# Kernel optimization log

Measured on AMD Instinct MI355X. Metric: run time of the kernel, lower is better.

The kernel has to match this reference:

```python
import jax, jax.numpy as jnp
import numpy as np

B, T, H, K = 128, 32, 256, 32


def setup_inputs() -> dict:
    key = jax.random.key(0)
    ks = jax.random.split(key, 24)
    s = 0.02  # small weight scale keeps exp(pdf) stable

    def n(k, shape, scale=s):
        return jax.random.normal(k, shape, dtype=jnp.float32) * scale

    inp = {
        "input_encoded": jax.random.normal(ks[0], (B, T, H), dtype=jnp.float32),
        "y_prev": jax.random.normal(ks[1], (B, T), dtype=jnp.float32),
        "attn_W1": n(ks[2], (H, 3 * H)),
        "attn_b1": n(ks[3], (H,)),
        "attn_W2": n(ks[4], (1, H)),
        "attn_b2": n(ks[5], (1,)),
        "fc_W": n(ks[6], (1, H + 1)),
        "fc_b": n(ks[7], (1,)),
        "var_W": n(ks[8], (H, H + 1)),
        "var_b": n(ks[9], (H,)),
        "W_ih": n(ks[10], (4 * H, 1)),
        "W_hh": n(ks[11], (4 * H, H)),
        "b_ih": n(ks[12], (4 * H,)),
        "b_hh": n(ks[13], (4 * H,)),
        "fc_dec_W": n(ks[14], (1, H)),
        "fc_dec_b": n(ks[15], (1,)),
        "pdf_W": n(ks[16], (1, H + 1)),
        "pdf_b": n(ks[17], (1,)),
        "fc_enc_W": n(ks[18], (1, H)),
        "fc_enc_b": n(ks[19], (1,)),
        "num_particles": K,
    }
    return inp


def reference(input_encoded, y_prev, attn_W1, attn_b1, attn_W2, attn_b2,
              fc_W, fc_b, var_W, var_b, W_ih, W_hh, b_ih, b_hh,
              fc_dec_W, fc_dec_b, pdf_W, pdf_b, fc_enc_W, fc_enc_b,
              num_particles):
    Bn, Tn, Hn = input_encoded.shape
    Kn = num_particles
    base = jax.random.key(42)
    arB = jnp.arange(Bn)

    def step(carry, xs):
        hiddens, cells = carry  # each (K*B, H), flat index = k*B + b
        t, y_t = xs  # y_t: (B,)
        k1, k2 = jax.random.split(jax.random.fold_in(base, t))
        # particle means (torch: mean over dim 0 of (K, B, H) view)
        hm = hiddens.reshape(Kn, Bn, Hn).mean(axis=0)  # (B, H)
        cm = cells.reshape(Kn, Bn, Hn).mean(axis=0)
        # attention over encoder timesteps
        x = jnp.concatenate([
            jnp.broadcast_to(hm[:, None, :], (Bn, Tn, Hn)),
            jnp.broadcast_to(cm[:, None, :], (Bn, Tn, Hn)),
            input_encoded], axis=2)  # (B, T, 3H)
        a = jnp.tanh(x @ attn_W1.T + attn_b1) @ attn_W2.T + attn_b2  # (B, T, 1)
        beta = jax.nn.softmax(a[..., 0], axis=1)  # (B, T)
        context = jnp.einsum('bt,bth->bh', beta, input_encoded)  # (B, H)
        y_tilde = jnp.concatenate([context, y_t[:, None]], axis=1) @ fc_W.T + fc_b  # (B, 1)
        var = jnp.concatenate([y_tilde, hm], axis=1) @ var_W.T + var_b  # (B, H)
        # single-step LSTM cell over all particles (torch gate order i,f,g,o)
        x_in = jnp.tile(y_tilde, (Kn, 1))  # (K*B, 1)
        gates = x_in @ W_ih.T + b_ih + hiddens @ W_hh.T + b_hh  # (K*B, 4H)
        i, f, g, o = jnp.split(gates, 4, axis=1)
        c_new = jax.nn.sigmoid(f) * cells + jax.nn.sigmoid(i) * jnp.tanh(g)
        h_new = jax.nn.sigmoid(o) * jnp.tanh(c_new)
        # reparameterization: h = mu + eps * softplus(var)
        std = jnp.tile(jax.nn.softplus(var), (Kn, 1))  # (K*B, H)
        eps = jax.random.normal(k1, (Kn * Bn, Hn), dtype=h_new.dtype)
        h_new = h_new + eps * std
        # sort_hidden: per-batch argsort of 1-d projection, gather hiddens only
        proj = h_new @ fc_dec_W.T + fc_dec_b  # (K*B, 1)
        idx = jnp.argsort(proj.reshape(Kn, Bn).T, axis=1)  # (B, K)
        flat = (arB[:, None] + idx * Bn).T.reshape(-1)  # (K*B,)
        h_sorted = h_new[flat]
        # particle weights (replicates torch's view(-1, K, 1) reshape exactly)
        y = jnp.concatenate([h_sorted, jnp.tile(y_tilde, (Kn, 1))], axis=1)
        prob = jnp.exp(y @ pdf_W.T + pdf_b).reshape(Bn, Kn, 1)
        prob = prob / prob.sum(axis=1, keepdims=True)
        # soft-resampling: multinomial over (B, K) rows (torch: prob.view(K,-1).T)
        logits = jnp.log(prob.reshape(Kn, Bn).T)  # (B, K)
        samp = jax.random.categorical(k2, logits, shape=(Kn, Bn))  # (K, B)
        flat2 = (samp * Bn + arB[None, :]).reshape(-1)
        return (h_sorted[flat2], c_new[flat2]), context

    h0 = jnp.zeros((Kn * Bn, Hn), dtype=input_encoded.dtype)
    (hiddens, _), contexts = jax.lax.scan(step, (h0, h0), (jnp.arange(Tn), y_prev.T))
    context = contexts[-1]
    hm = hiddens.reshape(Kn, Bn, Hn).mean(axis=0)  # (B, H)
    y_pred = hm @ fc_dec_W.T + fc_dec_b + context @ fc_enc_W.T + fc_enc_b  # (B, 1)
    return y_pred
```

## Files before the change

kernel.cpp:

```cpp
#include <hip/hip_runtime.h>
#include <cstdint>


#define Bn 128
#define Tn 32
#define Hn 256
#define Kn 32

__host__ __device__ inline void tf2x32(uint32_t k0, uint32_t k1, uint32_t x0, uint32_t x1,
                                       uint32_t &o0, uint32_t &o1) {
  uint32_t ks2 = k0 ^ k1 ^ 0x1BD11BDAu;
  x0 += k0; x1 += k1;
#define TFR(r) { x0 += x1; x1 = (x1 << r) | (x1 >> (32 - r)); x1 ^= x0; }
  TFR(13) TFR(15) TFR(26) TFR(6)
  x0 += k1;  x1 += ks2 + 1u;
  TFR(17) TFR(29) TFR(16) TFR(24)
  x0 += ks2; x1 += k0 + 2u;
  TFR(13) TFR(15) TFR(26) TFR(6)
  x0 += k0;  x1 += k1 + 3u;
  TFR(17) TFR(29) TFR(16) TFR(24)
  x0 += k1;  x1 += ks2 + 4u;
  TFR(13) TFR(15) TFR(26) TFR(6)
  x0 += ks2; x1 += k0 + 5u;
#undef TFR
  o0 = x0; o1 = x1;
}

__device__ __forceinline__ float erfinv_xla(float x) {
  float w = -log1pf(-x * x);
  float p;
  if (w < 5.0f) {
    w = w - 2.5f;
    p = 2.81022636e-08f;
    p = fmaf(p, w, 3.43273939e-07f);
    p = fmaf(p, w, -3.5233877e-06f);
    p = fmaf(p, w, -4.39150654e-06f);
    p = fmaf(p, w, 0.00021858087f);
    p = fmaf(p, w, -0.00125372503f);
    p = fmaf(p, w, -0.00417768164f);
    p = fmaf(p, w, 0.246640727f);
    p = fmaf(p, w, 1.50140941f);
  } else {
    w = sqrtf(w) - 3.0f;
    p = -0.000200214257f;
    p = fmaf(p, w, 0.000100950558f);
    p = fmaf(p, w, 0.00134934322f);
    p = fmaf(p, w, -0.00367342844f);
    p = fmaf(p, w, 0.00573950773f);
    p = fmaf(p, w, -0.0076224613f);
    p = fmaf(p, w, 0.00943887047f);
    p = fmaf(p, w, 1.00167406f);
    p = fmaf(p, w, 2.83297682f);
  }
  return p * x;
}

__device__ __forceinline__ float sigmoid_xla(float x) {
  return 0.5f + 0.5f * tanhf(0.5f * x);
}

__device__ __forceinline__ float u01_from_bits(uint32_t bits) {
  return __uint_as_float((bits >> 9) | 0x3F800000u) - 1.0f;
}

__device__ __forceinline__ float normal_from_idx(uint32_t ka, uint32_t kb, uint32_t idx) {
  uint32_t o0, o1; tf2x32(ka, kb, 0u, idx, o0, o1);
  float f = u01_from_bits(o0 ^ o1);
  const float LO = __uint_as_float(0xBF7FFFFFu);
  float u = fmaxf(LO, f * 2.0f + LO);
  return __uint_as_float(0x3FB504F3u) * erfinv_xla(u);
}

__device__ __forceinline__ float gumbel_from_idx(uint32_t ka, uint32_t kb, uint32_t idx) {
  uint32_t o0, o1; tf2x32(ka, kb, 0u, idx, o0, o1);
  float f = u01_from_bits(o0 ^ o1);
  const float TINY = __uint_as_float(0x00800000u);
  float u = fmaxf(TINY, f + TINY);
  return -logf(-logf(u));
}


__global__ void darnn_p0(const float* __restrict__ W1, const float* __restrict__ Whh,
                         const float* __restrict__ varW,
                         float* __restrict__ W1hT, float* __restrict__ W1cT,
                         float* __restrict__ W1eT, float* __restrict__ WhhT,
                         float* __restrict__ varWT) {
  int bid = blockIdx.x, tid = threadIdx.x;
  if (bid < 768) {
    int part = bid >> 8, j = bid & 255;
    float v = W1[tid * 768 + part * 256 + j];
    float* dst = (part == 0) ? W1hT : (part == 1) ? W1cT : W1eT;
    dst[j * 256 + tid] = v;
  } else if (bid < 1024) {
    int j = bid - 768;
    for (int idx = tid; idx < 1024; idx += 256) {
      int h = idx >> 2, q = idx & 3;
      WhhT[j * 1024 + idx] = Whh[(q * 256 + h) * 256 + j];
    }
  } else {
    int j2 = bid - 1024;
    varWT[j2 * 256 + tid] = varW[tid * 257 + j2];
  }
}

__global__ void darnn_p1(const float* __restrict__ enc, const float* __restrict__ W1eT,
                         const float* __restrict__ b1, float* __restrict__ encW1) {
  int bt = blockIdx.x, tid = threadIdx.x;
  __shared__ float se[256];
  se[tid] = enc[bt * 256 + tid];
  __syncthreads();
  float acc = 0.f;
  for (int j = 0; j < 256; ++j) acc = fmaf(se[j], W1eT[j * 256 + tid], acc);
  encW1[bt * 256 + tid] = acc + b1[tid];
}


__launch_bounds__(1024, 4)
__global__ void darnn_step(const float* __restrict__ enc, const float* __restrict__ yprev,
                           const float* __restrict__ W1hT, const float* __restrict__ W1cT,
                           const float* __restrict__ encW1, const float* __restrict__ W2,
                           const float* __restrict__ b2p, const float* __restrict__ fcW,
                           const float* __restrict__ fcbp, const float* __restrict__ varWT,
                           const float* __restrict__ varb, const float* __restrict__ WhhT,
                           const float* __restrict__ Wih, const float* __restrict__ bih,
                           const float* __restrict__ bhh, const float* __restrict__ decW,
                           const float* __restrict__ decbp, const float* __restrict__ pdfW,
                           const float* __restrict__ pdfbp,
                           const float* __restrict__ proj_p, const float* __restrict__ pdot_p,
                           const float* __restrict__ ytl_p,
                           const float* __restrict__ hprev, const float* __restrict__ cprev,
                           float* __restrict__ hcur, float* __restrict__ ccur,
                           float* __restrict__ proj_c, float* __restrict__ pdot_c,
                           float* __restrict__ ytl_c, float* __restrict__ ctx_g,
                           int t, uint32_t k1a, uint32_t k1b, uint32_t k2a, uint32_t k2b) {
  const int bid = blockIdx.x, tid = threadIdx.x;
  const int b = bid & 127, khalf = bid >> 7;
  const int bg = b >> 5, bloc = b & 31;
  const int h = tid & 255, kg = tid >> 8, lane = tid & 63;

  __shared__ __align__(16) float s_wbuf[8192];
  __shared__ __align__(16) float s_h[16 * 256];
  __shared__ float s_gp[1024], s_w[1024], s_gvals[1024];
  __shared__ int s_srck[1024];
  __shared__ float s_ytlp[32], s_den[32], s_logit[32];
  __shared__ int s_rowH[32], s_rowC[32];
  __shared__ __align__(16) float s_hm[256], s_cm[256], s_hmc[256], s_red[256], s_std[256];
  __shared__ float s_sc[32], s_beta[32];
  __shared__ float s_ytl;
  __shared__ float s_sredP[16 * 4], s_sredQ[16 * 4];

  const float4* W4 = (const float4*)WhhT;
  const int jp = tid >> 8;
  float4 rA = W4[jp * 256 + h];
  float4 rB = W4[(4 + jp) * 256 + h];

  if (t > 0) {
    if (tid < 32) s_ytlp[tid] = ytl_p[bg * 32 + tid];
    {
      int bl = tid >> 5, k = tid & 31;
      s_gp[tid] = proj_p[k * 128 + bg * 32 + bl];
    }
    __syncthreads();
    {
      int bl = tid >> 5, k = tid & 31;
      float p = s_gp[tid];
      const float* gp = s_gp + bl * 32;
      int rank = 0;
      for (int kk = 0; kk < 32; ++kk) {
        float q = gp[kk];
        rank += (q < p) || (q == p && kk < k);
      }
      s_srck[bl * 32 + rank] = k;
      float wv = expf((pdot_p[k * 128 + bg * 32 + bl] + s_ytlp[bl] * pdfW[256]) + pdfbp[0]);
      s_w[bl * 32 + rank] = wv;
    }
    __syncthreads();
    if (tid < 32) {
      float s = 0.f;
      for (int bl = 0; bl < 32; ++bl) s += s_w[bl * 32 + tid];
      s_den[tid] = s;
    }
    __syncthreads();
    if (tid < 32) s_logit[tid] = logf(s_w[bloc * 32 + tid] / s_den[tid]);
    __syncthreads();
    {
      int ko = tid >> 5, k = tid & 31, r2 = ko * 128 + b;
      s_gvals[tid] = gumbel_from_idx(k2a, k2b, (uint32_t)(r2 * 32 + k)) + s_logit[k];
    }
    __syncthreads();
    if (tid < 32) {
      int ko = tid;
      const float* gv = s_gvals + ko * 32;
      float best = gv[0];
      int sv = 0;
      for (int k = 1; k < 32; ++k) { float v = gv[k]; if (v > best) { best = v; sv = k; } }
      s_rowH[ko] = s_srck[bloc * 32 + sv] * 128 + b;
      s_rowC[ko] = sv * 128 + b;
    }
  } else {
    if (tid < 32) {
      s_rowH[tid] = tid * 128 + b;
      s_rowC[tid] = tid * 128 + b;
    }
  }
  __syncthreads();

  if (tid < 256) {
    float s1 = 0.f;
    for (int k0 = 0; k0 < 32; k0 += 8) {
      float hv[8];
#pragma unroll
      for (int i = 0; i < 8; ++i) hv[i] = hprev[(size_t)s_rowH[k0 + i] * 256 + tid];
#pragma unroll
      for (int i = 0; i < 8; ++i) s1 += hv[i];
    }
    s_hm[tid] = s1 * 0.03125f;
  } else if (tid < 512) {
    int j = tid & 255;
    float s2 = 0.f;
    for (int k0 = 0; k0 < 32; k0 += 8) {
      float cv[8];
#pragma unroll
      for (int i = 0; i < 8; ++i) cv[i] = cprev[(size_t)s_rowC[k0 + i] * 256 + j];
#pragma unroll
      for (int i = 0; i < 8; ++i) s2 += cv[i];
    }
    s_cm[j] = s2 * 0.03125f;
  } else {
    int i = tid - 512;
    int rr = i >> 6, c4 = i & 63;
    const float4* hp4 = (const float4*)hprev;
    float4* sh4 = (float4*)s_h;
    sh4[i]       = hp4[(size_t)s_rowH[khalf * 16 + rr] * 64 + c4];
    sh4[i + 512] = hp4[(size_t)s_rowH[khalf * 16 + 8 + rr] * 64 + c4];
  }
  __syncthreads();

  if (tid < 256) {
    float acc = 0.f;
    for (int j0 = 0; j0 < 256; j0 += 8) {
      float wh[8], wc[8];
#pragma unroll
      for (int i = 0; i < 8; ++i) {
        wh[i] = W1hT[(j0 + i) * 256 + tid];
        wc[i] = W1cT[(j0 + i) * 256 + tid];
      }
#pragma unroll
      for (int i = 0; i < 8; ++i) {
        acc = fmaf(s_hm[j0 + i], wh[i], acc);
        acc = fmaf(s_cm[j0 + i], wc[i], acc);
      }
    }
    s_hmc[tid] = acc;
  }
  __syncthreads();

  {
    int wv = tid >> 6;
    for (int tt = wv * 2; tt < wv * 2 + 2; ++tt) {
      float p = 0.f;
      for (int hh = lane; hh < 256; hh += 64)
        p += tanhf(encW1[(b * 32 + tt) * 256 + hh] + s_hmc[hh]) * W2[hh];
      for (int off = 32; off; off >>= 1) p += __shfl_down(p, off);
      if (lane == 0) s_sc[tt] = p + b2p[0];
    }
  }
  __syncthreads();
  if (tid == 0) {
    float m = s_sc[0];
    for (int k = 1; k < 32; ++k) m = fmaxf(m, s_sc[k]);
    float s = 0.f;
    for (int k = 0; k < 32; ++k) { float e = expf(s_sc[k] - m); s_beta[k] = e; s += e; }
    for (int k = 0; k < 32; ++k) s_beta[k] /= s;
  }
  __syncthreads();
  if (tid < 256) {
    float cx = 0.f;
    for (int tt = 0; tt < 32; ++tt) cx = fmaf(s_beta[tt], enc[(b * 32 + tt) * 256 + tid], cx);
    if (khalf == 0) ctx_g[b * 256 + tid] = cx;
    s_red[tid] = cx * fcW[tid];
  }
  __syncthreads();
  if (tid == 0) {
    const float4* r4 = (const float4*)s_red;
    float s = 0.f;
    for (int i = 0; i < 64; ++i) {
      float4 v = r4[i];
      s = s + v.x; s = s + v.y; s = s + v.z; s = s + v.w;
    }
    s += yprev[b * 32 + t] * fcW[256];
    s_ytl = s + fcbp[0];
    if (khalf == 0) ytl_c[b] = s_ytl;
  }
  __syncthreads();
  if (tid < 256) {
    float v = s_ytl * varWT[tid];
    for (int j0 = 0; j0 < 256; j0 += 16) {
      float wv[16];
#pragma unroll
      for (int i = 0; i < 16; ++i) wv[i] = varWT[(1 + j0 + i) * 256 + tid];
#pragma unroll
      for (int i = 0; i < 16; ++i) v = fmaf(s_hm[j0 + i], wv[i], v);
    }
    v += varb[tid];
    s_std[tid] = fmaxf(v, 0.f) + log1pf(expf(-fabsf(v)));
  }

  float ai[4], af[4], ag[4], ao[4];
#pragma unroll
  for (int r = 0; r < 4; ++r) { ai[r] = af[r] = ag[r] = ao[r] = 0.f; }
  {
    float4* wb4 = (float4*)s_wbuf;
    const float* shr = s_h + (kg * 4) * 256;
    for (int it = 0; it < 32; ++it) {
      __syncthreads();
      wb4[tid] = rA;
      wb4[tid + 1024] = rB;
      if (it + 1 < 32) {
        rA = W4[((it + 1) * 8 + jp) * 256 + h];
        rB = W4[((it + 1) * 8 + 4 + jp) * 256 + h];
      }
      __syncthreads();
      int j0 = it * 8;
#pragma unroll
      for (int g = 0; g < 2; ++g) {
        const float4* wg = (const float4*)s_wbuf + (g ? 1024 : 0) + h;
        float4 w0 = wg[0];
        float4 w1 = wg[256];
        float4 w2 = wg[512];
        float4 w3 = wg[768];
        int j = j0 + g * 4;
#pragma unroll
        for (int r = 0; r < 4; ++r) {
          float4 h4 = *(const float4*)(shr + r * 256 + j);
          ai[r] = fmaf(h4.x, w0.x, ai[r]); ai[r] = fmaf(h4.y, w1.x, ai[r]);
          ai[r] = fmaf(h4.z, w2.x, ai[r]); ai[r] = fmaf(h4.w, w3.x, ai[r]);
          af[r] = fmaf(h4.x, w0.y, af[r]); af[r] = fmaf(h4.y, w1.y, af[r]);
          af[r] = fmaf(h4.z, w2.y, af[r]); af[r] = fmaf(h4.w, w3.y, af[r]);
          ag[r] = fmaf(h4.x, w0.z, ag[r]); ag[r] = fmaf(h4.y, w1.z, ag[r]);
          ag[r] = fmaf(h4.z, w2.z, ag[r]); ag[r] = fmaf(h4.w, w3.z, ag[r]);
          ao[r] = fmaf(h4.x, w0.w, ao[r]); ao[r] = fmaf(h4.y, w1.w, ao[r]);
          ao[r] = fmaf(h4.z, w2.w, ao[r]); ao[r] = fmaf(h4.w, w3.w, ao[r]);
        }
      }
    }
  }
  __syncthreads();

  const float bI = bih[h], bF = bih[256 + h], bG = bih[512 + h], bO = bih[768 + h];
  const float dI = bhh[h], dF = bhh[256 + h], dG = bhh[512 + h], dO = bhh[768 + h];
  const float wI = Wih[h], wF = Wih[256 + h], wG = Wih[512 + h], wO = Wih[768 + h];
  float hnv[4];
#pragma unroll
  for (int r = 0; r < 4; ++r) {
    int rl = kg * 4 + r;
    int k = khalf * 16 + rl, R = k * 128 + b;
    float xb = s_ytl;
    float pi = ((xb * wI + bI) + ai[r]) + dI;
    float pf = ((xb * wF + bF) + af[r]) + dF;
    float pg = ((xb * wG + bG) + ag[r]) + dG;
    float po = ((xb * wO + bO) + ao[r]) + dO;
    float c_old = cprev[(size_t)s_rowC[k] * 256 + h];
    float cn = sigmoid_xla(pf) * c_old + sigmoid_xla(pi) * tanhf(pg);
    float hn = sigmoid_xla(po) * tanhf(cn);
    float eps = normal_from_idx(k1a, k1b, (uint32_t)(R * 256 + h));
    hn = hn + eps * s_std[h];
    ccur[(size_t)R * 256 + h] = cn;
    hcur[(size_t)R * 256 + h] = hn;
    hnv[r] = hn;
  }

  const float dw = decW[h], pw = pdfW[h];
#pragma unroll
  for (int r = 0; r < 4; ++r) {
    int rl = kg * 4 + r;
    float v = hnv[r] * dw;
    for (int off = 32; off; off >>= 1) v += __shfl_down(v, off);
    if (lane == 0) s_sredP[rl * 4 + (h >> 6)] = v;
    float v2 = hnv[r] * pw;
    for (int off = 32; off; off >>= 1) v2 += __shfl_down(v2, off);
    if (lane == 0) s_sredQ[rl * 4 + (h >> 6)] = v2;
  }
  __syncthreads();
  if (tid < 16) {
    int rl = tid, k = khalf * 16 + rl;
    proj_c[k * 128 + b] = ((s_sredP[rl * 4 + 0] + s_sredP[rl * 4 + 1]) +
                           (s_sredP[rl * 4 + 2] + s_sredP[rl * 4 + 3])) + decbp[0];
  } else if (tid < 32) {
    int rl = tid - 16, k = khalf * 16 + rl;
    pdot_c[k * 128 + b] = (s_sredQ[rl * 4 + 0] + s_sredQ[rl * 4 + 1]) +
                          (s_sredQ[rl * 4 + 2] + s_sredQ[rl * 4 + 3]);
  }
}


__launch_bounds__(256)
__global__ void darnn_kout(const float* __restrict__ proj_g, const float* __restrict__ pdot_g,
                           const float* __restrict__ ytl_prev, const float* __restrict__ hprev,
                           const float* __restrict__ ctx_g, const float* __restrict__ decW,
                           const float* __restrict__ decbp, const float* __restrict__ encWo,
                           const float* __restrict__ encbo, const float* __restrict__ pdfW,
                           const float* __restrict__ pdfbp,
                           uint32_t k2a, uint32_t k2b, float* __restrict__ out) {
  const int b = blockIdx.x, tid = threadIdx.x, bg = b >> 5, bloc = b & 31;
  const int lane = tid & 63;
  __shared__ float s_gp[1024], s_w[1024];
  __shared__ int s_srck[1024];
  __shared__ float s_ytlp[32], s_den[32], s_logit[32];
  __shared__ int s_row[32];
  __shared__ float s_hm[256], s_sred[8];

  if (tid < 32) s_ytlp[tid] = ytl_prev[bg * 32 + tid];
  for (int i = tid; i < 1024; i += 256) {
    int bl = i >> 5, k = i & 31;
    s_gp[i] = proj_g[k * 128 + bg * 32 + bl];
  }
  __syncthreads();
  for (int i = tid; i < 1024; i += 256) {
    int bl = i >> 5, k = i & 31;
    float p = s_gp[i];
    const float* gp = s_gp + bl * 32;
    int rank = 0;
    for (int kk = 0; kk < 32; ++kk) {
      float q = gp[kk];
      rank += (q < p) || (q == p && kk < k);
    }
    s_srck[bl * 32 + rank] = k;
    float wv = expf((pdot_g[k * 128 + bg * 32 + bl] + s_ytlp[bl] * pdfW[256]) + pdfbp[0]);
    s_w[bl * 32 + rank] = wv;
  }
  __syncthreads();
  if (tid < 32) {
    float s = 0.f;
    for (int bl = 0; bl < 32; ++bl) s += s_w[bl * 32 + tid];
    s_den[tid] = s;
  }
  __syncthreads();
  if (tid < 32) s_logit[tid] = logf(s_w[bloc * 32 + tid] / s_den[tid]);
  __syncthreads();
  if (tid < 32) {
    int ko = tid, r2 = ko * 128 + b;
    float best = gumbel_from_idx(k2a, k2b, (uint32_t)(r2 * 32)) + s_logit[0];
    int sv = 0;
    for (int k = 1; k < 32; ++k) {
      float v = gumbel_from_idx(k2a, k2b, (uint32_t)(r2 * 32 + k)) + s_logit[k];
      if (v > best) { best = v; sv = k; }
    }
    s_row[ko] = s_srck[bloc * 32 + sv] * 128 + b;
  }
  __syncthreads();
  {
    float s1 = 0.f;
    for (int k = 0; k < 32; ++k) s1 += hprev[(size_t)s_row[k] * 256 + tid];
    s_hm[tid] = s1 * 0.03125f;
  }
  __syncthreads();
  {
    int wvi = tid >> 6;
    float v1 = s_hm[tid] * decW[tid];
    float v2 = ctx_g[b * 256 + tid] * encWo[tid];
    for (int off = 32; off; off >>= 1) { v1 += __shfl_down(v1, off); v2 += __shfl_down(v2, off); }
    if (lane == 0) { s_sred[wvi] = v1; s_sred[4 + wvi] = v2; }
  }
  __syncthreads();
  if (tid == 0) {
    float d1 = (s_sred[0] + s_sred[1]) + (s_sred[2] + s_sred[3]);
    float d2 = (s_sred[4] + s_sred[5]) + (s_sred[6] + s_sred[7]);
    out[b] = ((d1 + decbp[0]) + d2) + encbo[0];
  }
}

extern "C" void kernel_launch(void* const* d_in, const int* in_sizes, int n_in,
                              void* d_out, int out_size, void* d_ws, size_t ws_size,
                              hipStream_t stream) {
  const float* enc   = (const float*)d_in[0];
  const float* yprev = (const float*)d_in[1];
  const float* W1    = (const float*)d_in[2];
  const float* b1    = (const float*)d_in[3];
  const float* W2    = (const float*)d_in[4];
  const float* b2    = (const float*)d_in[5];
  const float* fcW   = (const float*)d_in[6];
  const float* fcb   = (const float*)d_in[7];
  const float* varW  = (const float*)d_in[8];
  const float* varb  = (const float*)d_in[9];
  const float* Wih   = (const float*)d_in[10];
  const float* Whh   = (const float*)d_in[11];
  const float* bih   = (const float*)d_in[12];
  const float* bhh   = (const float*)d_in[13];
  const float* decW  = (const float*)d_in[14];
  const float* decb  = (const float*)d_in[15];
  const float* pdfW  = (const float*)d_in[16];
  const float* pdfb  = (const float*)d_in[17];
  const float* encWo = (const float*)d_in[18];
  const float* encbo = (const float*)d_in[19];

  float* ws = (float*)d_ws;
  size_t o = 0;
  float* encW1 = ws + o; o += (size_t)Bn * Tn * Hn;
  float* W1hT  = ws + o; o += (size_t)Hn * Hn;
  float* W1cT  = ws + o; o += (size_t)Hn * Hn;
  float* W1eT  = ws + o; o += (size_t)Hn * Hn;
  float* WhhT  = ws + o; o += (size_t)Hn * 4 * Hn;
  float* varWT = ws + o; o += (size_t)257 * Hn;
  float* hbuf0 = ws + o; o += (size_t)Kn * Bn * Hn;
  float* hbuf1 = ws + o; o += (size_t)Kn * Bn * Hn;
  float* cbuf0 = ws + o; o += (size_t)Kn * Bn * Hn;
  float* cbuf1 = ws + o; o += (size_t)Kn * Bn * Hn;
  float* ytl0  = ws + o; o += 128;
  float* ytl1  = ws + o; o += 128;
  float* ctx_g = ws + o; o += (size_t)Bn * Hn;
  float* proj0 = ws + o; o += 4096;
  float* proj1 = ws + o; o += 4096;
  float* pdot0 = ws + o; o += 4096;
  float* pdot1 = ws + o; o += 4096;
  if (ws_size < o * sizeof(float)) return;

  float* hb[2] = { hbuf0, hbuf1 };
  float* cb[2] = { cbuf0, cbuf1 };
  float* yb[2] = { ytl0, ytl1 };
  float* pp[2] = { proj0, proj1 };
  float* pq[2] = { pdot0, pdot1 };

  hipMemsetAsync(hbuf1, 0, (size_t)Kn * Bn * Hn * sizeof(float), stream);
  hipMemsetAsync(cbuf1, 0, (size_t)Kn * Bn * Hn * sizeof(float), stream);

  darnn_p0<<<1281, 256, 0, stream>>>(W1, Whh, varW, W1hT, W1cT, W1eT, WhhT, varWT);
  darnn_p1<<<Bn * Tn, 256, 0, stream>>>(enc, W1eT, b1, encW1);

  uint32_t k2pa = 0, k2pb = 0;
  for (int t = 0; t < Tn; ++t) {
    uint32_t f0, f1, k1a, k1b, k2a, k2b;
    tf2x32(0u, 42u, 0u, (uint32_t)t, f0, f1);
    tf2x32(f0, f1, 0u, 0u, k1a, k1b);
    tf2x32(f0, f1, 0u, 1u, k2a, k2b);
    int cur = t & 1, prv = (t + 1) & 1;

    darnn_step<<<2 * Bn, 1024, 0, stream>>>(enc, yprev, W1hT, W1cT, encW1, W2, b2,
                                            fcW, fcb, varWT, varb, WhhT, Wih, bih, bhh,
                                            decW, decb, pdfW, pdfb,
                                            pp[prv], pq[prv], yb[prv], hb[prv], cb[prv],
                                            hb[cur], cb[cur], pp[cur], pq[cur], yb[cur],
                                            ctx_g, t, k1a, k1b, k2pa, k2pb);
    k2pa = k2a; k2pb = k2b;
  }

  darnn_kout<<<Bn, 256, 0, stream>>>(pp[1], pq[1], yb[1], hb[1], ctx_g,
                                     decW, decb, encWo, encbo, pdfW, pdfb,
                                     k2pa, k2pb, (float*)d_out);
}
```

Baseline: 2.533 ms.

## Process all 32 particles per batch block, halving grid and removing duplicated attention work

Each step kernel block now handles all 32 particles of a batch element instead of 16, so the grid shrinks from 256 to 128 blocks. The attention, context, and variance computations were repeated in both half-blocks, and that duplication goes away. Each thread now accumulates 8 rows of LSTM gates, which doubles register accumulators and shared memory for the hidden state. The cost is only 128 blocks on a 256-CU device, which lowers parallelism, and higher register pressure.

After: 4.038 ms. +59.4%, slower.

```diff
diff --git a/kernel.cpp b/kernel.cpp
--- a/kernel.cpp
+++ b/kernel.cpp
@@ -133,13 +133,12 @@
                            float* __restrict__ proj_c, float* __restrict__ pdot_c,
                            float* __restrict__ ytl_c, float* __restrict__ ctx_g,
                            int t, uint32_t k1a, uint32_t k1b, uint32_t k2a, uint32_t k2b) {
-  const int bid = blockIdx.x, tid = threadIdx.x;
-  const int b = bid & 127, khalf = bid >> 7;
+  const int b = blockIdx.x, tid = threadIdx.x;
   const int bg = b >> 5, bloc = b & 31;
   const int h = tid & 255, kg = tid >> 8, lane = tid & 63;
 
   __shared__ __align__(16) float s_wbuf[8192];
-  __shared__ __align__(16) float s_h[16 * 256];
+  __shared__ __align__(16) float s_h[32 * 256];
   __shared__ float s_gp[1024], s_w[1024], s_gvals[1024];
   __shared__ int s_srck[1024];
   __shared__ float s_ytlp[32], s_den[32], s_logit[32];
@@ -147,7 +146,7 @@
   __shared__ __align__(16) float s_hm[256], s_cm[256], s_hmc[256], s_red[256], s_std[256];
   __shared__ float s_sc[32], s_beta[32];
   __shared__ float s_ytl;
-  __shared__ float s_sredP[16 * 4], s_sredQ[16 * 4];
+  __shared__ float s_sredP[32 * 4], s_sredQ[32 * 4];
 
   const float4* W4 = (const float4*)WhhT;
   const int jp = tid >> 8;
@@ -227,12 +226,15 @@
     }
     s_cm[j] = s2 * 0.03125f;
   } else {
-    int i = tid - 512;
-    int rr = i >> 6, c4 = i & 63;
+    int base = tid - 512;
     const float4* hp4 = (const float4*)hprev;
     float4* sh4 = (float4*)s_h;
-    sh4[i]       = hp4[(size_t)s_rowH[khalf * 16 + rr] * 64 + c4];
-    sh4[i + 512] = hp4[(size_t)s_rowH[khalf * 16 + 8 + rr] * 64 + c4];
+#pragma unroll
+    for (int ii = 0; ii < 4; ++ii) {
+      int i = base + ii * 512;
+      int rr = i >> 6, c4 = i & 63;
+      sh4[i] = hp4[(size_t)s_rowH[rr] * 64 + c4];
+    }
   }
   __syncthreads();
 
@@ -277,7 +279,7 @@
   if (tid < 256) {
     float cx = 0.f;
     for (int tt = 0; tt < 32; ++tt) cx = fmaf(s_beta[tt], enc[(b * 32 + tt) * 256 + tid], cx);
-    if (khalf == 0) ctx_g[b * 256 + tid] = cx;
+    ctx_g[b * 256 + tid] = cx;
     s_red[tid] = cx * fcW[tid];
   }
   __syncthreads();
@@ -290,7 +292,7 @@
     }
     s += yprev[b * 32 + t] * fcW[256];
     s_ytl = s + fcbp[0];
-    if (khalf == 0) ytl_c[b] = s_ytl;
+    ytl_c[b] = s_ytl;
   }
   __syncthreads();
   if (tid < 256) {
@@ -306,12 +308,12 @@
     s_std[tid] = fmaxf(v, 0.f) + log1pf(expf(-fabsf(v)));
   }
 
-  float ai[4], af[4], ag[4], ao[4];
-#pragma unroll
-  for (int r = 0; r < 4; ++r) { ai[r] = af[r] = ag[r] = ao[r] = 0.f; }
+  float ai[8], af[8], ag[8], ao[8];
+#pragma unroll
+  for (int r = 0; r < 8; ++r) { ai[r] = af[r] = ag[r] = ao[r] = 0.f; }
   {
     float4* wb4 = (float4*)s_wbuf;
-    const float* shr = s_h + (kg * 4) * 256;
+    const float* shr = s_h + (kg * 8) * 256;
     for (int it = 0; it < 32; ++it) {
       __syncthreads();
       wb4[tid] = rA;
@@ -331,7 +333,7 @@
         float4 w3 = wg[768];
         int j = j0 + g * 4;
 #pragma unroll
-        for (int r = 0; r < 4; ++r) {
+        for (int r = 0; r < 8; ++r) {
           float4 h4 = *(const float4*)(shr + r * 256 + j);
           ai[r] = fmaf(h4.x, w0.x, ai[r]); ai[r] = fmaf(h4.y, w1.x, ai[r]);
           ai[r] = fmaf(h4.z, w2.x, ai[r]); ai[r] = fmaf(h4.w, w3.x, ai[r]);
@@ -350,18 +352,19 @@
   const float bI = bih[h], bF = bih[256 + h], bG = bih[512 + h], bO = bih[768 + h];
   const float dI = bhh[h], dF = bhh[256 + h], dG = bhh[512 + h], dO = bhh[768 + h];
   const float wI = Wih[h], wF = Wih[256 + h], wG = Wih[512 + h], wO = Wih[768 + h];
-  float hnv[4];
-#pragma unroll
-  for (int r = 0; r < 4; ++r) {
-    int rl = kg * 4 + r;
-    int k = khalf * 16 + rl, R = k * 128 + b;
+  float c_old8[8];
+#pragma unroll
+  for (int r = 0; r < 8; ++r) c_old8[r] = cprev[(size_t)s_rowC[kg * 8 + r] * 256 + h];
+  float hnv[8];
+#pragma unroll
+  for (int r = 0; r < 8; ++r) {
+    int k = kg * 8 + r, R = k * 128 + b;
     float xb = s_ytl;
     float pi = ((xb * wI + bI) + ai[r]) + dI;
     float pf = ((xb * wF + bF) + af[r]) + dF;
     float pg = ((xb * wG + bG) + ag[r]) + dG;
     float po = ((xb * wO + bO) + ao[r]) + dO;
-    float c_old = cprev[(size_t)s_rowC[k] * 256 + h];
-    float cn = sigmoid_xla(pf) * c_old + sigmoid_xla(pi) * tanhf(pg);
+    float cn = sigmoid_xla(pf) * c_old8[r] + sigmoid_xla(pi) * tanhf(pg);
     float hn = sigmoid_xla(po) * tanhf(cn);
     float eps = normal_from_idx(k1a, k1b, (uint32_t)(R * 256 + h));
     hn = hn + eps * s_std[h];
@@ -372,8 +375,8 @@
 
   const float dw = decW[h], pw = pdfW[h];
 #pragma unroll
-  for (int r = 0; r < 4; ++r) {
-    int rl = kg * 4 + r;
+  for (int r = 0; r < 8; ++r) {
+    int rl = kg * 8 + r;
     float v = hnv[r] * dw;
     for (int off = 32; off; off >>= 1) v += __shfl_down(v, off);
     if (lane == 0) s_sredP[rl * 4 + (h >> 6)] = v;
@@ -382,14 +385,14 @@
     if (lane == 0) s_sredQ[rl * 4 + (h >> 6)] = v2;
   }
   __syncthreads();
-  if (tid < 16) {
-    int rl = tid, k = khalf * 16 + rl;
-    proj_c[k * 128 + b] = ((s_sredP[rl * 4 + 0] + s_sredP[rl * 4 + 1]) +
-                           (s_sredP[rl * 4 + 2] + s_sredP[rl * 4 + 3])) + decbp[0];
-  } else if (tid < 32) {
-    int rl = tid - 16, k = khalf * 16 + rl;
-    pdot_c[k * 128 + b] = (s_sredQ[rl * 4 + 0] + s_sredQ[rl * 4 + 1]) +
-                          (s_sredQ[rl * 4 + 2] + s_sredQ[rl * 4 + 3]);
+  if (tid < 32) {
+    int k = tid;
+    proj_c[k * 128 + b] = ((s_sredP[k * 4 + 0] + s_sredP[k * 4 + 1]) +
+                           (s_sredP[k * 4 + 2] + s_sredP[k * 4 + 3])) + decbp[0];
+  } else if (tid < 64) {
+    int k = tid - 32;
+    pdot_c[k * 128 + b] = (s_sredQ[k * 4 + 0] + s_sredQ[k * 4 + 1]) +
+                          (s_sredQ[k * 4 + 2] + s_sredQ[k * 4 + 3]);
   }
 }
 
@@ -535,12 +538,12 @@
     tf2x32(f0, f1, 0u, 1u, k2a, k2b);
     int cur = t & 1, prv = (t + 1) & 1;
 
-    darnn_step<<<2 * Bn, 1024, 0, stream>>>(enc, yprev, W1hT, W1cT, encW1, W2, b2,
-                                            fcW, fcb, varWT, varb, WhhT, Wih, bih, bhh,
-                                            decW, decb, pdfW, pdfb,
-                                            pp[prv], pq[prv], yb[prv], hb[prv], cb[prv],
-                                            hb[cur], cb[cur], pp[cur], pq[cur], yb[cur],
-                                            ctx_g, t, k1a, k1b, k2pa, k2pb);
+    darnn_step<<<Bn, 1024, 0, stream>>>(enc, yprev, W1hT, W1cT, encW1, W2, b2,
+                                        fcW, fcb, varWT, varb, WhhT, Wih, bih, bhh,
+                                        decW, decb, pdfW, pdfb,
+                                        pp[prv], pq[prv], yb[prv], hb[prv], cb[prv],
+                                        hb[cur], cb[cur], pp[cur], pq[cur], yb[cur],
+                                        ctx_g, t, k1a, k1b, k2pa, k2pb);
     k2pa = k2a; k2pb = k2b;
   }
 
```

## Double-buffer W_hh tiles in LDS via direct global-to-LDS DMA loads

Applied to the files above, without the earlier changes.

Replaces the register-staged prefetch of W_hh tiles with `global_load_lds` DMA into two alternating LDS buffers. This removes one barrier per iteration and the register round-trip, so the next tile's load overlaps the current tile's FMAs. It also vectorizes the serial softmax and context-reduction reads from LDS, and hoists the c_prev gathers ahead of the gate math. The extra 32KB of LDS may reduce occupancy, and correctness depends on the barrier waiting for outstanding DMA loads.

Measured after the change: 2.666 ms. +5.3%, slower.

```diff
diff --git a/kernel.cpp b/kernel.cpp
--- a/kernel.cpp
+++ b/kernel.cpp
@@ -6,6 +6,12 @@
 #define Tn 32
 #define Hn 256
 #define Kn 32
+
+__device__ __forceinline__ void dma16(const float4* g, float4* l) {
+  __builtin_amdgcn_global_load_lds(
+      (const __attribute__((address_space(1))) void*)g,
+      (__attribute__((address_space(3))) void*)l, 16, 0, 0);
+}
 
 __host__ __device__ inline void tf2x32(uint32_t k0, uint32_t k1, uint32_t x0, uint32_t x1,
                                        uint32_t &o0, uint32_t &o1) {
@@ -138,7 +144,8 @@
   const int bg = b >> 5, bloc = b & 31;
   const int h = tid & 255, kg = tid >> 8, lane = tid & 63;
 
-  __shared__ __align__(16) float s_wbuf[8192];
+  __shared__ __align__(16) float s_wbufA[8192];
+  __shared__ __align__(16) float s_wbufB[8192];
   __shared__ __align__(16) float s_h[16 * 256];
   __shared__ float s_gp[1024], s_w[1024], s_gvals[1024];
   __shared__ int s_srck[1024];
@@ -150,9 +157,8 @@
   __shared__ float s_sredP[16 * 4], s_sredQ[16 * 4];
 
   const float4* W4 = (const float4*)WhhT;
-  const int jp = tid >> 8;
-  float4 rA = W4[jp * 256 + h];
-  float4 rB = W4[(4 + jp) * 256 + h];
+  dma16(W4 + tid, (float4*)s_wbufA + tid);
+  dma16(W4 + 1024 + tid, (float4*)s_wbufA + 1024 + tid);
 
   if (t > 0) {
     if (tid < 32) s_ytlp[tid] = ytl_p[bg * 32 + tid];
@@ -267,10 +273,20 @@
   }
   __syncthreads();
   if (tid == 0) {
-    float m = s_sc[0];
-    for (int k = 1; k < 32; ++k) m = fmaxf(m, s_sc[k]);
+    float sc[32];
+    const float4* c4p = (const float4*)s_sc;
+    float4 v4[8];
+#pragma unroll
+    for (int i = 0; i < 8; ++i) v4[i] = c4p[i];
+#pragma unroll
+    for (int i = 0; i < 8; ++i) {
+      sc[i * 4 + 0] = v4[i].x; sc[i * 4 + 1] = v4[i].y;
+      sc[i * 4 + 2] = v4[i].z; sc[i * 4 + 3] = v4[i].w;
+    }
+    float m = sc[0];
+    for (int k = 1; k < 32; ++k) m = fmaxf(m, sc[k]);
     float s = 0.f;
-    for (int k = 0; k < 32; ++k) { float e = expf(s_sc[k] - m); s_beta[k] = e; s += e; }
+    for (int k = 0; k < 32; ++k) { float e = expf(sc[k] - m); s_beta[k] = e; s += e; }
     for (int k = 0; k < 32; ++k) s_beta[k] /= s;
   }
   __syncthreads();
@@ -284,9 +300,14 @@
   if (tid == 0) {
     const float4* r4 = (const float4*)s_red;
     float s = 0.f;
-    for (int i = 0; i < 64; ++i) {
-      float4 v = r4[i];
-      s = s + v.x; s = s + v.y; s = s + v.z; s = s + v.w;
+    for (int i0 = 0; i0 < 64; i0 += 16) {
+      float4 v[16];
+#pragma unroll
+      for (int i = 0; i < 16; ++i) v[i] = r4[i0 + i];
+#pragma unroll
+      for (int i = 0; i < 16; ++i) {
+        s = s + v[i].x; s = s + v[i].y; s = s + v[i].z; s = s + v[i].w;
+      }
     }
     s += yprev[b * 32 + t] * fcW[256];
     s_ytl = s + fcbp[0];
@@ -310,21 +331,20 @@
 #pragma unroll
   for (int r = 0; r < 4; ++r) { ai[r] = af[r] = ag[r] = ao[r] = 0.f; }
   {
-    float4* wb4 = (float4*)s_wbuf;
     const float* shr = s_h + (kg * 4) * 256;
     for (int it = 0; it < 32; ++it) {
       __syncthreads();
-      wb4[tid] = rA;
-      wb4[tid + 1024] = rB;
       if (it + 1 < 32) {
-        rA = W4[((it + 1) * 8 + jp) * 256 + h];
-        rB = W4[((it + 1) * 8 + 4 + jp) * 256 + h];
+        const float4* gn = W4 + (it + 1) * 2048;
+        float4* dst = ((it + 1) & 1) ? (float4*)s_wbufB : (float4*)s_wbufA;
+        dma16(gn + tid, dst + tid);
+        dma16(gn + 1024 + tid, dst + 1024 + tid);
       }
-      __syncthreads();
+      const float* wt = (it & 1) ? s_wbufB : s_wbufA;
       int j0 = it * 8;
 #pragma unroll
       for (int g = 0; g < 2; ++g) {
-        const float4* wg = (const float4*)s_wbuf + (g ? 1024 : 0) + h;
+        const float4* wg = (const float4*)wt + (g ? 1024 : 0) + h;
         float4 w0 = wg[0];
         float4 w1 = wg[256];
         float4 w2 = wg[512];
@@ -350,6 +370,10 @@
   const float bI = bih[h], bF = bih[256 + h], bG = bih[512 + h], bO = bih[768 + h];
   const float dI = bhh[h], dF = bhh[256 + h], dG = bhh[512 + h], dO = bhh[768 + h];
   const float wI = Wih[h], wF = Wih[256 + h], wG = Wih[512 + h], wO = Wih[768 + h];
+  float c_old4[4];
+#pragma unroll
+  for (int r = 0; r < 4; ++r)
+    c_old4[r] = cprev[(size_t)s_rowC[khalf * 16 + kg * 4 + r] * 256 + h];
   float hnv[4];
 #pragma unroll
   for (int r = 0; r < 4; ++r) {
@@ -360,8 +384,7 @@
     float pf = ((xb * wF + bF) + af[r]) + dF;
     float pg = ((xb * wG + bG) + ag[r]) + dG;
     float po = ((xb * wO + bO) + ao[r]) + dO;
-    float c_old = cprev[(size_t)s_rowC[k] * 256 + h];
-    float cn = sigmoid_xla(pf) * c_old + sigmoid_xla(pi) * tanhf(pg);
+    float cn = sigmoid_xla(pf) * c_old4[r] + sigmoid_xla(pi) * tanhf(pg);
     float hn = sigmoid_xla(po) * tanhf(cn);
     float eps = normal_from_idx(k1a, k1b, (uint32_t)(R * 256 + h));
     hn = hn + eps * s_std[h];
```
